# Kernel tuning notes

Measured on AMD Instinct MI355X. Metric: run time of the kernel, lower is better.

Reference implementation:

```python
import jax, jax.numpy as jnp
import numpy as np

DIM = 1024
E = 8
TOP_K = 2
HID = int(DIM * 2.68)  # 2744


def setup_inputs() -> dict:
    key = jax.random.key(0)
    ks = jax.random.split(key, 8)
    s = 0.02
    return {
        "x": jax.random.normal(ks[0], (4, 1024, DIM), dtype=jnp.float32),
        "gate_w": jax.random.normal(ks[1], (E, DIM), dtype=jnp.float32) * s,
        "w1": jax.random.normal(ks[2], (E, HID, DIM), dtype=jnp.float32) * s,
        "w2": jax.random.normal(ks[3], (E, HID, DIM), dtype=jnp.float32) * s,
        "w3": jax.random.normal(ks[4], (E, DIM, HID), dtype=jnp.float32) * s,
        "sw1": jax.random.normal(ks[5], (HID, DIM), dtype=jnp.float32) * s,
        "sw2": jax.random.normal(ks[6], (HID, DIM), dtype=jnp.float32) * s,
        "sw3": jax.random.normal(ks[7], (DIM, HID), dtype=jnp.float32) * s,
    }


def reference(x, gate_w, w1, w2, w3, sw1, sw2, sw3):
    B, T, C = x.shape
    xf = x.reshape(-1, C)  # [S, C]
    logits = xf @ gate_w.T  # [S, E]
    rw = jax.nn.softmax(logits.astype(jnp.float32), axis=-1)
    tkw, tki = jax.lax.top_k(rw, TOP_K)  # [S, K]
    nE = rw.shape[-1]
    importance = rw.mean(0)  # [E]
    load = jax.nn.one_hot(tki[:, 0], nE, dtype=jnp.float32).mean(0)  # [E]
    aux_loss = nE * (importance * load).sum()
    tkw = tkw / tkw.sum(-1, keepdims=True)
    tkw = tkw.astype(x.dtype)
    # dense all-expert SwiGLU (faithful to original: every expert on every token)
    h = jax.nn.silu(jnp.einsum('sc,ehc->seh', xf, w1)) * jnp.einsum('sc,ehc->seh', xf, w2)  # [S,E,H]
    eo = jnp.einsum('seh,ech->sec', h, w3)  # [S, E, C]
    sel = jnp.take_along_axis(eo, tki[:, :, None], axis=1)  # [S, K, C]
    weighted = (sel * tkw[:, :, None]).sum(1)  # [S, C]
    shared = (jax.nn.silu(xf @ sw1.T) * (xf @ sw2.T)) @ sw3.T  # [S, C]
    y = (weighted + shared).reshape(B, T, C)
    return y, aux_loss
```

## Files before the change

kernel.cpp:

```cpp
#include <hip/hip_runtime.h>
#include <cstdio>
#include <cstdint>

#define S_TOK 4096
#define CDIM  1024
#define EXP   8
#define HRAW  2744
#define HPAD  2816
#define MAXROWS  13312
#define MAXTILES 104
#define NSLICE1  (HPAD / 128)
#define NSLICE2  (CDIM / 256)
#define G1_BLKS  (MAXTILES * NSLICE1)

typedef __attribute__((ext_vector_type(8))) short bf16x8;
typedef __attribute__((ext_vector_type(4))) float f32x4;
typedef __attribute__((ext_vector_type(4))) unsigned short us4;
typedef __attribute__((ext_vector_type(8))) unsigned short us8;
typedef unsigned short us;

__device__ __forceinline__ us f2bf(float f) {
  unsigned u = __float_as_uint(f);
  u += 0x7fffu + ((u >> 16) & 1u);
  return (us)(u >> 16);
}
__device__ __forceinline__ float bf2f(us v) {
  return __uint_as_float((unsigned)v << 16);
}

__device__ __forceinline__ void gl16(const us* g, us* l) {
  __builtin_amdgcn_global_load_lds((__attribute__((address_space(1))) void*)g,
                                   (__attribute__((address_space(3))) void*)l,
                                   16, 0, 0);
}

__device__ __forceinline__ int xcd_swz(int orig, int nwg) {
  int q = nwg >> 3, r = nwg & 7;
  int x = orig & 7, idx = orig >> 3;
  return (x < r ? x * (q + 1) : r * (q + 1) + (x - r) * q) + idx;
}

#define CH8_RP1  (HPAD * CDIM / 8)
#define CH8_CPR  (HPAD / 8)

__device__ __forceinline__ void cvt8_rowpad(const float* __restrict__ src,
                                            us* __restrict__ dst, int idx) {
  int m = idx / CH8_RP1, rem = idx - m * CH8_RP1;
  int r = rem >> 7, c8 = rem & 127;
  us8 o;
  if (r < HRAW) {
    const float4* p = (const float4*)(src + ((size_t)(m * HRAW + r) * CDIM + c8 * 8));
    float4 v0 = p[0], v1 = p[1];
    o[0] = f2bf(v0.x); o[1] = f2bf(v0.y); o[2] = f2bf(v0.z); o[3] = f2bf(v0.w);
    o[4] = f2bf(v1.x); o[5] = f2bf(v1.y); o[6] = f2bf(v1.z); o[7] = f2bf(v1.w);
  } else {
    o[0] = 0; o[1] = 0; o[2] = 0; o[3] = 0; o[4] = 0; o[5] = 0; o[6] = 0; o[7] = 0;
  }
  *(us8*)(dst + ((size_t)(m * HPAD + r) * CDIM + c8 * 8)) = o;
}

__device__ __forceinline__ void cvt8_colpad(const float* __restrict__ src,
                                            us* __restrict__ dst, int idx) {
  int r = idx / CH8_CPR, c8 = idx - r * CH8_CPR;
  int c = c8 * 8;
  us8 o;
  if (c < HRAW) {
    const float4* p = (const float4*)(src + (size_t)r * HRAW + c);
    float4 v0 = p[0], v1 = p[1];
    o[0] = f2bf(v0.x); o[1] = f2bf(v0.y); o[2] = f2bf(v0.z); o[3] = f2bf(v0.w);
    o[4] = f2bf(v1.x); o[5] = f2bf(v1.y); o[6] = f2bf(v1.z); o[7] = f2bf(v1.w);
  } else {
    o[0] = 0; o[1] = 0; o[2] = 0; o[3] = 0; o[4] = 0; o[5] = 0; o[6] = 0; o[7] = 0;
  }
  *(us8*)(dst + (size_t)r * HPAD + c) = o;
}

#define GATE_BLKS 1024
#define CVT_BLKS  2048
#define AB8_W1   (8 * CH8_RP1)
#define AB8_W2   (AB8_W1 + 8 * CH8_RP1)
#define AB8_SW1  (AB8_W2 + CH8_RP1)
#define AB8_SW2  (AB8_SW1 + CH8_RP1)

__global__ void __launch_bounds__(256) cvtgate_kernel(
    const float* __restrict__ x, const float* __restrict__ gw,
    const float* __restrict__ w1, const float* __restrict__ w2,
    const float* __restrict__ sw1, const float* __restrict__ sw2,
    us* __restrict__ xb, us* __restrict__ w1b, us* __restrict__ w2b,
    us* __restrict__ sw1b, us* __restrict__ sw2b,
    int* __restrict__ tki, float* __restrict__ tkw, float* __restrict__ probs) {
  if (blockIdx.x < GATE_BLKS) {
    const int wv = threadIdx.x >> 6, lane = threadIdx.x & 63;
    const int s = blockIdx.x * 4 + wv;
    const float4* xs4 = (const float4*)(x + (size_t)s * CDIM);
    float acc[8] = {0, 0, 0, 0, 0, 0, 0, 0};
#pragma unroll
    for (int j = 0; j < 4; j++) {
      float4 v = xs4[lane * 4 + j];
      int c = lane * 16 + j * 4;
      us4 ov;
      ov.x = f2bf(v.x); ov.y = f2bf(v.y); ov.z = f2bf(v.z); ov.w = f2bf(v.w);
      *(us4*)(xb + (size_t)s * CDIM + c) = ov;
#pragma unroll
      for (int ee = 0; ee < 8; ee++) {
        const float* g = gw + ee * CDIM + c;
        acc[ee] += v.x * g[0] + v.y * g[1] + v.z * g[2] + v.w * g[3];
      }
    }
#pragma unroll
    for (int ee = 0; ee < 8; ee++) {
#pragma unroll
      for (int off = 32; off > 0; off >>= 1) acc[ee] += __shfl_xor(acc[ee], off, 64);
    }
    if (lane == 0) {
      float mx = acc[0];
      for (int ee = 1; ee < 8; ee++) mx = fmaxf(mx, acc[ee]);
      float p[8], sm = 0.f;
      for (int ee = 0; ee < 8; ee++) { p[ee] = expf(acc[ee] - mx); sm += p[ee]; }
      float inv = 1.f / sm;
      for (int ee = 0; ee < 8; ee++) probs[s * 8 + ee] = p[ee] * inv;
      int i0 = 0; float b0 = p[0];
      for (int ee = 1; ee < 8; ee++) if (p[ee] > b0) { b0 = p[ee]; i0 = ee; }
      int i1 = -1; float b1 = -1.f;
      for (int ee = 0; ee < 8; ee++) if (ee != i0 && p[ee] > b1) { b1 = p[ee]; i1 = ee; }
      float rw0 = b0 * inv, rw1 = b1 * inv;
      float den = 1.f / (rw0 + rw1);
      tki[2 * s] = i0; tki[2 * s + 1] = i1;
      tkw[2 * s] = rw0 * den; tkw[2 * s + 1] = rw1 * den;
    }
    return;
  }
  for (int i = (blockIdx.x - GATE_BLKS) * 256 + threadIdx.x; i < AB8_SW2;
       i += CVT_BLKS * 256) {
    if (i < AB8_W1)       cvt8_rowpad(w1,  w1b,  i);
    else if (i < AB8_W2)  cvt8_rowpad(w2,  w2b,  i - AB8_W1);
    else if (i < AB8_SW1) cvt8_rowpad(sw1, sw1b, i - AB8_W2);
    else                  cvt8_rowpad(sw2, sw2b, i - AB8_SW1);
  }
}

__global__ void __launch_bounds__(512) build_kernel(const int* __restrict__ tki,
                                                    const float* __restrict__ tkw,
                                                    const float* __restrict__ probs,
                                                    int* __restrict__ meta,
                                                    int* __restrict__ pairtok,
                                                    float* __restrict__ pairw,
                                                    int* __restrict__ invmap,
                                                    int* __restrict__ tile_expert,
                                                    float* __restrict__ aux_out) {
  const int tid = threadIdx.x, lane = tid & 63, wv = tid >> 6;
  __shared__ int s_cnt[EXP];
  __shared__ int s_amc[EXP];
  __shared__ float s_imp[EXP];
  {
    const int e = wv;
    int c_cnt = 0, c_amc = 0;
    float imp = 0.f;
    for (int s0 = 0; s0 < S_TOK; s0 += 64) {
      int s = s0 + lane;
      int i0 = tki[2 * s], i1 = tki[2 * s + 1];
      c_cnt += (i0 == e) || (i1 == e);
      c_amc += (i0 == e);
      imp += probs[s * 8 + e];
    }
#pragma unroll
    for (int off = 32; off > 0; off >>= 1) {
      c_cnt += __shfl_xor(c_cnt, off, 64);
      c_amc += __shfl_xor(c_amc, off, 64);
      imp   += __shfl_xor(imp, off, 64);
    }
    if (lane == 0) { s_cnt[e] = c_cnt; s_amc[e] = c_amc; s_imp[e] = imp; }
  }
  __syncthreads();
  int pad[EXP], start[EXP];
  int o = S_TOK;
#pragma unroll
  for (int j = 0; j < EXP; j++) {
    pad[j] = ((s_cnt[j] + 127) >> 7) << 7;
    start[j] = o;
    o += pad[j];
  }
  const int total = o;
  for (int r = tid; r < S_TOK; r += 512) { pairtok[r] = r; pairw[r] = 1.f; }
  {
    const int e = wv;
    int base = start[e];
    for (int s0 = 0; s0 < S_TOK; s0 += 64) {
      int s = s0 + lane;
      int i0 = tki[2 * s], i1 = tki[2 * s + 1];
      bool m0 = (i0 == e), m1 = (i1 == e);
      bool mm = m0 || m1;
      unsigned long long mk = __ballot(mm);
      if (mm) {
        int pos = base + __popcll(mk & ((1ull << lane) - 1ull));
        pairtok[pos] = s;
        pairw[pos] = m0 ? tkw[2 * s] : tkw[2 * s + 1];
        invmap[2 * s + (m0 ? 0 : 1)] = pos;
      }
      base += __popcll(mk);
    }
    for (int r = base + lane; r < start[e] + pad[e]; r += 64) {
      pairtok[r] = -1; pairw[r] = 0.f;
    }
  }
  if (tid < 128) {
    int ex = 8;
    if (tid >= 32) {
      int rr = tid * 128;
#pragma unroll
      for (int j = 0; j < EXP; j++)
        if (rr >= start[j] && rr < start[j] + pad[j]) ex = j;
    }
    tile_expert[tid] = ex;
  }
  if (tid == 0) {
    meta[0] = total >> 7;
    float a = 0.f;
    for (int j = 0; j < EXP; j++)
      a += (s_imp[j] * (1.f / 4096.f)) * ((float)s_amc[j] * (1.f / 4096.f));
    aux_out[0] = 8.f * a;
  }
}

#define W3CVT_BLKS 1024
#define W38_CHUNKS (8 * CDIM * CH8_CPR)
#define W38_TOT    (W38_CHUNKS + CDIM * CH8_CPR)

__global__ void __launch_bounds__(256, 2) gemm1_kernel(
    const us* __restrict__ xb, const us* __restrict__ w1b, const us* __restrict__ w2b,
    const us* __restrict__ sw1b, const us* __restrict__ sw2b,
    const int* __restrict__ pairtok, const int* __restrict__ tile_expert,
    const int* __restrict__ meta, us* __restrict__ h,
    const float* __restrict__ w3, const float* __restrict__ sw3,
    us* __restrict__ w3b, us* __restrict__ sw3b) {
  if (blockIdx.x >= G1_BLKS) {
    for (int i = (blockIdx.x - G1_BLKS) * 256 + threadIdx.x; i < W38_TOT;
         i += W3CVT_BLKS * 256) {
      if (i < W38_CHUNKS) cvt8_colpad(w3,  w3b,  i);
      else                cvt8_colpad(sw3, sw3b, i - W38_CHUNKS);
    }
    return;
  }
  const int wgid = xcd_swz(blockIdx.x, G1_BLKS);
  const int mt = wgid % MAXTILES;
  if (mt >= meta[0]) return;
  const int n0 = (wgid / MAXTILES) * 128;
  const int e = tile_expert[mt];
  const us* B1 = (e == 8) ? sw1b : (w1b + (size_t)e * HPAD * CDIM);
  const us* B2 = (e == 8) ? sw2b : (w2b + (size_t)e * HPAD * CDIM);
  const int row0 = mt * 128;
  __shared__ __align__(16) us sA[128 * 64];
  __shared__ __align__(16) us sB1[128 * 64];
  __shared__ __align__(16) us sB2[128 * 64];
  const int tid = threadIdx.x, lane = tid & 63;
  const int wm = tid >> 7, wn = (tid >> 6) & 1;
  const int srow = tid >> 3;
  const int soct = (tid & 7) ^ (srow & 7);
  const us* gA[4];
  const us* gB1a[4];
  const us* gB2a[4];
#pragma unroll
  for (int j = 0; j < 4; j++) {
    int t = pairtok[row0 + j * 32 + srow]; if (t < 0) t = 0;
    gA[j]   = xb + (size_t)t * CDIM + soct * 8;
    gB1a[j] = B1 + (size_t)(n0 + j * 32 + srow) * CDIM + soct * 8;
    gB2a[j] = B2 + (size_t)(n0 + j * 32 + srow) * CDIM + soct * 8;
  }
  f32x4 au[4][4], av[4][4];
#pragma unroll
  for (int m = 0; m < 4; m++)
#pragma unroll
    for (int n = 0; n < 4; n++)
#pragma unroll
      for (int r = 0; r < 4; r++) { au[m][n][r] = 0.f; av[m][n][r] = 0.f; }

  const int rl = lane & 15, fo = lane >> 4;
  const int x0 = ((0 + fo) ^ (rl & 7)) << 3;
  const int x1 = ((4 + fo) ^ (rl & 7)) << 3;
  for (int k0 = 0; k0 < CDIM; k0 += 64) {
#pragma unroll
    for (int j = 0; j < 4; j++) {
      gl16(gA[j] + k0,   &sA[(j * 256 + tid) * 8]);
      gl16(gB1a[j] + k0, &sB1[(j * 256 + tid) * 8]);
      gl16(gB2a[j] + k0, &sB2[(j * 256 + tid) * 8]);
    }
    __syncthreads();
#pragma unroll
    for (int ks = 0; ks < 2; ks++) {
      const int kx = ks ? x1 : x0;
      bf16x8 a[4], b1[4], b2[4];
#pragma unroll
      for (int m = 0; m < 4; m++)
        a[m] = *(const bf16x8*)&sA[(wm * 64 + m * 16 + rl) * 64 + kx];
#pragma unroll
      for (int n = 0; n < 4; n++) {
        b1[n] = *(const bf16x8*)&sB1[(wn * 64 + n * 16 + rl) * 64 + kx];
        b2[n] = *(const bf16x8*)&sB2[(wn * 64 + n * 16 + rl) * 64 + kx];
      }
#pragma unroll
      for (int m = 0; m < 4; m++)
#pragma unroll
        for (int n = 0; n < 4; n++) {
          au[m][n] = __builtin_amdgcn_mfma_f32_16x16x32_bf16(a[m], b1[n], au[m][n], 0, 0, 0);
          av[m][n] = __builtin_amdgcn_mfma_f32_16x16x32_bf16(a[m], b2[n], av[m][n], 0, 0, 0);
        }
    }
    __syncthreads();
  }
  const int rb = (lane >> 4) * 4, cb = lane & 15;
#pragma unroll
  for (int m = 0; m < 4; m++)
#pragma unroll
    for (int n = 0; n < 4; n++)
#pragma unroll
      for (int r = 0; r < 4; r++) {
        int row = row0 + wm * 64 + m * 16 + rb + r;
        int col = n0 + wn * 64 + n * 16 + cb;
        float u = au[m][n][r], v = av[m][n][r];
        float sg = 1.f / (1.f + __expf(-u));
        h[(size_t)row * HPAD + col] = f2bf(u * sg * v);
      }
}

__global__ void __launch_bounds__(256, 2) gemm2_kernel(
    const us* __restrict__ h, const us* __restrict__ w3b, const us* __restrict__ sw3b,
    const int* __restrict__ tile_expert, const int* __restrict__ meta,
    us* __restrict__ eo) {
  const int wgid = xcd_swz(blockIdx.x, MAXTILES * NSLICE2);
  const int mt = wgid % MAXTILES;
  if (mt >= meta[0]) return;
  const int n0 = (wgid / MAXTILES) * 256;
  const int e = tile_expert[mt];
  const us* B = (e == 8) ? sw3b : (w3b + (size_t)e * CDIM * HPAD);
  const int row0 = mt * 128;
  __shared__ __align__(16) us sA[128 * 64];
  __shared__ __align__(16) us sB[256 * 64];
  const int tid = threadIdx.x, lane = tid & 63;
  const int wm = tid >> 7, wn = (tid >> 6) & 1;
  const int srow = tid >> 3;
  const int soct = (tid & 7) ^ (srow & 7);
  const us* gA[4];
  const us* gB[8];
#pragma unroll
  for (int j = 0; j < 4; j++)
    gA[j] = h + (size_t)(row0 + j * 32 + srow) * HPAD + soct * 8;
#pragma unroll
  for (int j = 0; j < 8; j++)
    gB[j] = B + (size_t)(n0 + j * 32 + srow) * HPAD + soct * 8;
  f32x4 ac[4][8];
#pragma unroll
  for (int m = 0; m < 4; m++)
#pragma unroll
    for (int n = 0; n < 8; n++)
#pragma unroll
      for (int r = 0; r < 4; r++) ac[m][n][r] = 0.f;

  const int rl = lane & 15, fo = lane >> 4;
  const int x0 = ((0 + fo) ^ (rl & 7)) << 3;
  const int x1 = ((4 + fo) ^ (rl & 7)) << 3;
  for (int k0 = 0; k0 < HPAD; k0 += 64) {
#pragma unroll
    for (int j = 0; j < 4; j++)
      gl16(gA[j] + k0, &sA[(j * 256 + tid) * 8]);
#pragma unroll
    for (int j = 0; j < 8; j++)
      gl16(gB[j] + k0, &sB[(j * 256 + tid) * 8]);
    __syncthreads();
#pragma unroll
    for (int ks = 0; ks < 2; ks++) {
      const int kx = ks ? x1 : x0;
      bf16x8 a[4], b[8];
#pragma unroll
      for (int m = 0; m < 4; m++)
        a[m] = *(const bf16x8*)&sA[(wm * 64 + m * 16 + rl) * 64 + kx];
#pragma unroll
      for (int n = 0; n < 8; n++)
        b[n] = *(const bf16x8*)&sB[(wn * 128 + n * 16 + rl) * 64 + kx];
#pragma unroll
      for (int m = 0; m < 4; m++)
#pragma unroll
        for (int n = 0; n < 8; n++)
          ac[m][n] = __builtin_amdgcn_mfma_f32_16x16x32_bf16(a[m], b[n], ac[m][n], 0, 0, 0);
    }
    __syncthreads();
  }
  const int rb = (lane >> 4) * 4, cb = lane & 15;
#pragma unroll
  for (int m = 0; m < 4; m++)
#pragma unroll
    for (int n = 0; n < 8; n++)
#pragma unroll
      for (int r = 0; r < 4; r++) {
        int row = row0 + wm * 64 + m * 16 + rb + r;
        int col = n0 + wn * 128 + n * 16 + cb;
        eo[(size_t)row * CDIM + col] = f2bf(ac[m][n][r]);
      }
}

__global__ void __launch_bounds__(256) combine_kernel(const us* __restrict__ eo,
                                                      const int* __restrict__ invmap,
                                                      const float* __restrict__ pairw,
                                                      float* __restrict__ out) {
  const int s = blockIdx.x;
  const int c = threadIdx.x * 4;
  const int j0 = invmap[2 * s], j1 = invmap[2 * s + 1];
  const float w0 = pairw[j0], w1 = pairw[j1];
  us4 a = *(const us4*)(eo + (size_t)s * CDIM + c);
  us4 b = *(const us4*)(eo + (size_t)j0 * CDIM + c);
  us4 d = *(const us4*)(eo + (size_t)j1 * CDIM + c);
  float4 o;
  o.x = bf2f(a.x) + w0 * bf2f(b.x) + w1 * bf2f(d.x);
  o.y = bf2f(a.y) + w0 * bf2f(b.y) + w1 * bf2f(d.y);
  o.z = bf2f(a.z) + w0 * bf2f(b.z) + w1 * bf2f(d.z);
  o.w = bf2f(a.w) + w0 * bf2f(b.w) + w1 * bf2f(d.w);
  *(float4*)(out + (size_t)s * CDIM + c) = o;
}

extern "C" void kernel_launch(void* const* d_in, const int* in_sizes, int n_in,
                              void* d_out, int out_size, void* d_ws, size_t ws_size,
                              hipStream_t stream) {
  const float* x   = (const float*)d_in[0];
  const float* gw  = (const float*)d_in[1];
  const float* w1  = (const float*)d_in[2];
  const float* w2  = (const float*)d_in[3];
  const float* w3  = (const float*)d_in[4];
  const float* sw1 = (const float*)d_in[5];
  const float* sw2 = (const float*)d_in[6];
  const float* sw3 = (const float*)d_in[7];
  float* out = (float*)d_out;
  char* ws = (char*)d_ws;
  size_t off = 0;
  auto take = [&](size_t bytes) -> char* {
    char* p = ws + off;
    off = (off + bytes + 255) & ~(size_t)255;
    return p;
  };
  us* xb    = (us*)take((size_t)S_TOK * CDIM * 2);
  us* w1b   = (us*)take((size_t)EXP * HPAD * CDIM * 2);
  us* w2b   = (us*)take((size_t)EXP * HPAD * CDIM * 2);
  us* w3b   = (us*)take((size_t)EXP * CDIM * HPAD * 2);
  us* sw1b  = (us*)take((size_t)HPAD * CDIM * 2);
  us* sw2b  = (us*)take((size_t)HPAD * CDIM * 2);
  us* sw3b  = (us*)take((size_t)CDIM * HPAD * 2);
  us* hbuf  = (us*)take((size_t)MAXROWS * HPAD * 2);
  us* eo    = (us*)take((size_t)MAXROWS * CDIM * 2);
  int* pairtok = (int*)take(MAXROWS * 4);
  float* pairw = (float*)take(MAXROWS * 4);
  int* invmap  = (int*)take(S_TOK * 2 * 4);
  int* tile_expert = (int*)take(128 * 4);
  int* tki = (int*)take(S_TOK * 2 * 4);
  float* tkw = (float*)take(S_TOK * 2 * 4);
  float* probs = (float*)take(S_TOK * EXP * 4);
  int* meta = (int*)take(256);
  if (off > ws_size) {
    fprintf(stderr, "MoE kernel: ws too small, need %zu got %zu\n", off, ws_size);
    return;
  }
  cvtgate_kernel<<<GATE_BLKS + CVT_BLKS, 256, 0, stream>>>(
      x, gw, w1, w2, sw1, sw2, xb, w1b, w2b, sw1b, sw2b, tki, tkw, probs);
  build_kernel<<<1, 512, 0, stream>>>(tki, tkw, probs, meta, pairtok, pairw, invmap,
                                      tile_expert, out + (size_t)S_TOK * CDIM);
  gemm1_kernel<<<G1_BLKS + W3CVT_BLKS, 256, 0, stream>>>(
      xb, w1b, w2b, sw1b, sw2b, pairtok, tile_expert, meta, hbuf,
      w3, sw3, w3b, sw3b);
  gemm2_kernel<<<MAXTILES * NSLICE2, 256, 0, stream>>>(
      hbuf, w3b, sw3b, tile_expert, meta, eo);
  combine_kernel<<<S_TOK, 256, 0, stream>>>(eo, invmap, pairw, out);
}
```

Baseline: 409.4 us.

## Double-buffer gemm2 with 256x256 tiles and overlap routing build with weight conversion

Splits gating into its own kernel and folds the single-block routing build into the weight-conversion kernel, so the build runs alongside conversion instead of as a serial launch. Expert segments are now padded to 256 rows, so gemm2 can use 512-thread blocks with 256x256 tiles and double-buffered LDS that prefetches the next K slice while MFMAs run, with priority hints. Both GEMMs now skip tiles whose first row is padding. Larger padding adds wasted rows and more workspace, and the bigger gemm2 tile yields fewer blocks, which may lower occupancy.

```diff
diff --git a/kernel.cpp b/kernel.cpp
--- a/kernel.cpp
+++ b/kernel.cpp
@@ -7,11 +7,13 @@
 #define EXP   8
 #define HRAW  2744
 #define HPAD  2816
-#define MAXROWS  13312
-#define MAXTILES 104
+#define MAXROWS  14336
+#define MAXTILES 112
+#define MAXT2    56
 #define NSLICE1  (HPAD / 128)
-#define NSLICE2  (CDIM / 256)
 #define G1_BLKS  (MAXTILES * NSLICE1)
+#define G2_BLKS  (MAXT2 * 4)
+#define NT2K     (HPAD / 64)
 
 typedef __attribute__((ext_vector_type(8))) short bf16x8;
 typedef __attribute__((ext_vector_type(4))) float f32x4;
@@ -75,150 +77,149 @@
   *(us8*)(dst + (size_t)r * HPAD + c) = o;
 }
 
-#define GATE_BLKS 1024
-#define CVT_BLKS  2048
+__global__ void __launch_bounds__(256) gate_kernel(const float* __restrict__ x,
+                                                   const float* __restrict__ gw,
+                                                   us* __restrict__ xb,
+                                                   int* __restrict__ tki,
+                                                   float* __restrict__ tkw,
+                                                   float* __restrict__ probs) {
+  const int wv = threadIdx.x >> 6, lane = threadIdx.x & 63;
+  const int s = blockIdx.x * 4 + wv;
+  const float4* xs4 = (const float4*)(x + (size_t)s * CDIM);
+  float acc[8] = {0, 0, 0, 0, 0, 0, 0, 0};
+#pragma unroll
+  for (int j = 0; j < 4; j++) {
+    float4 v = xs4[lane * 4 + j];
+    int c = lane * 16 + j * 4;
+    us4 ov;
+    ov.x = f2bf(v.x); ov.y = f2bf(v.y); ov.z = f2bf(v.z); ov.w = f2bf(v.w);
+    *(us4*)(xb + (size_t)s * CDIM + c) = ov;
+#pragma unroll
+    for (int ee = 0; ee < 8; ee++) {
+      const float* g = gw + ee * CDIM + c;
+      acc[ee] += v.x * g[0] + v.y * g[1] + v.z * g[2] + v.w * g[3];
+    }
+  }
+#pragma unroll
+  for (int ee = 0; ee < 8; ee++) {
+#pragma unroll
+    for (int off = 32; off > 0; off >>= 1) acc[ee] += __shfl_xor(acc[ee], off, 64);
+  }
+  if (lane == 0) {
+    float mx = acc[0];
+    for (int ee = 1; ee < 8; ee++) mx = fmaxf(mx, acc[ee]);
+    float p[8], sm = 0.f;
+    for (int ee = 0; ee < 8; ee++) { p[ee] = expf(acc[ee] - mx); sm += p[ee]; }
+    float inv = 1.f / sm;
+    for (int ee = 0; ee < 8; ee++) probs[s * 8 + ee] = p[ee] * inv;
+    int i0 = 0; float b0 = p[0];
+    for (int ee = 1; ee < 8; ee++) if (p[ee] > b0) { b0 = p[ee]; i0 = ee; }
+    int i1 = -1; float b1 = -1.f;
+    for (int ee = 0; ee < 8; ee++) if (ee != i0 && p[ee] > b1) { b1 = p[ee]; i1 = ee; }
+    float rw0 = b0 * inv, rw1 = b1 * inv;
+    float den = 1.f / (rw0 + rw1);
+    tki[2 * s] = i0; tki[2 * s + 1] = i1;
+    tkw[2 * s] = rw0 * den; tkw[2 * s + 1] = rw1 * den;
+  }
+}
+
+#define CVTAB_BLKS 2048
 #define AB8_W1   (8 * CH8_RP1)
 #define AB8_W2   (AB8_W1 + 8 * CH8_RP1)
 #define AB8_SW1  (AB8_W2 + CH8_RP1)
 #define AB8_SW2  (AB8_SW1 + CH8_RP1)
 
-__global__ void __launch_bounds__(256) cvtgate_kernel(
-    const float* __restrict__ x, const float* __restrict__ gw,
+__global__ void __launch_bounds__(512) cvtab_build_kernel(
     const float* __restrict__ w1, const float* __restrict__ w2,
     const float* __restrict__ sw1, const float* __restrict__ sw2,
-    us* __restrict__ xb, us* __restrict__ w1b, us* __restrict__ w2b,
+    us* __restrict__ w1b, us* __restrict__ w2b,
     us* __restrict__ sw1b, us* __restrict__ sw2b,
-    int* __restrict__ tki, float* __restrict__ tkw, float* __restrict__ probs) {
-  if (blockIdx.x < GATE_BLKS) {
-    const int wv = threadIdx.x >> 6, lane = threadIdx.x & 63;
-    const int s = blockIdx.x * 4 + wv;
-    const float4* xs4 = (const float4*)(x + (size_t)s * CDIM);
-    float acc[8] = {0, 0, 0, 0, 0, 0, 0, 0};
-#pragma unroll
-    for (int j = 0; j < 4; j++) {
-      float4 v = xs4[lane * 4 + j];
-      int c = lane * 16 + j * 4;
-      us4 ov;
-      ov.x = f2bf(v.x); ov.y = f2bf(v.y); ov.z = f2bf(v.z); ov.w = f2bf(v.w);
-      *(us4*)(xb + (size_t)s * CDIM + c) = ov;
-#pragma unroll
-      for (int ee = 0; ee < 8; ee++) {
-        const float* g = gw + ee * CDIM + c;
-        acc[ee] += v.x * g[0] + v.y * g[1] + v.z * g[2] + v.w * g[3];
-      }
-    }
-#pragma unroll
-    for (int ee = 0; ee < 8; ee++) {
-#pragma unroll
-      for (int off = 32; off > 0; off >>= 1) acc[ee] += __shfl_xor(acc[ee], off, 64);
-    }
-    if (lane == 0) {
-      float mx = acc[0];
-      for (int ee = 1; ee < 8; ee++) mx = fmaxf(mx, acc[ee]);
-      float p[8], sm = 0.f;
-      for (int ee = 0; ee < 8; ee++) { p[ee] = expf(acc[ee] - mx); sm += p[ee]; }
-      float inv = 1.f / sm;
-      for (int ee = 0; ee < 8; ee++) probs[s * 8 + ee] = p[ee] * inv;
-      int i0 = 0; float b0 = p[0];
-      for (int ee = 1; ee < 8; ee++) if (p[ee] > b0) { b0 = p[ee]; i0 = ee; }
-      int i1 = -1; float b1 = -1.f;
-      for (int ee = 0; ee < 8; ee++) if (ee != i0 && p[ee] > b1) { b1 = p[ee]; i1 = ee; }
-      float rw0 = b0 * inv, rw1 = b1 * inv;
-      float den = 1.f / (rw0 + rw1);
-      tki[2 * s] = i0; tki[2 * s + 1] = i1;
-      tkw[2 * s] = rw0 * den; tkw[2 * s + 1] = rw1 * den;
+    const int* __restrict__ tki, const float* __restrict__ tkw,
+    const float* __restrict__ probs, int* __restrict__ meta,
+    int* __restrict__ pairtok, float* __restrict__ pairw,
+    int* __restrict__ invmap, int* __restrict__ tile_expert,
+    float* __restrict__ aux_out) {
+  if (blockIdx.x == 0) {
+    const int tid = threadIdx.x, lane = tid & 63, wv = tid >> 6;
+    __shared__ int s_cnt[EXP];
+    __shared__ int s_amc[EXP];
+    __shared__ float s_imp[EXP];
+    {
+      const int e = wv;
+      int c_cnt = 0, c_amc = 0;
+      float imp = 0.f;
+      for (int s0 = 0; s0 < S_TOK; s0 += 64) {
+        int s = s0 + lane;
+        int i0 = tki[2 * s], i1 = tki[2 * s + 1];
+        c_cnt += (i0 == e) || (i1 == e);
+        c_amc += (i0 == e);
+        imp += probs[s * 8 + e];
+      }
+#pragma unroll
+      for (int off = 32; off > 0; off >>= 1) {
+        c_cnt += __shfl_xor(c_cnt, off, 64);
+        c_amc += __shfl_xor(c_amc, off, 64);
+        imp   += __shfl_xor(imp, off, 64);
+      }
+      if (lane == 0) { s_cnt[e] = c_cnt; s_amc[e] = c_amc; s_imp[e] = imp; }
+    }
+    __syncthreads();
+    int pad[EXP], start[EXP];
+    int o = S_TOK;
+#pragma unroll
+    for (int j = 0; j < EXP; j++) {
+      pad[j] = ((s_cnt[j] + 255) >> 8) << 8;
+      start[j] = o;
+      o += pad[j];
+    }
+    const int total = o;
+    for (int r = tid; r < S_TOK; r += 512) { pairtok[r] = r; pairw[r] = 1.f; }
+    {
+      const int e = wv;
+      int base = start[e];
+      for (int s0 = 0; s0 < S_TOK; s0 += 64) {
+        int s = s0 + lane;
+        int i0 = tki[2 * s], i1 = tki[2 * s + 1];
+        bool m0 = (i0 == e), m1 = (i1 == e);
+        bool mm = m0 || m1;
+        unsigned long long mk = __ballot(mm);
+        if (mm) {
+          int pos = base + __popcll(mk & ((1ull << lane) - 1ull));
+          pairtok[pos] = s;
+          pairw[pos] = m0 ? tkw[2 * s] : tkw[2 * s + 1];
+          invmap[2 * s + (m0 ? 0 : 1)] = pos;
+        }
+        base += __popcll(mk);
+      }
+      for (int r = base + lane; r < start[e] + pad[e]; r += 64) {
+        pairtok[r] = -1; pairw[r] = 0.f;
+      }
+    }
+    if (tid < 128) {
+      int ex = 8;
+      if (tid >= 32) {
+        int rr = tid * 128;
+#pragma unroll
+        for (int j = 0; j < EXP; j++)
+          if (rr >= start[j] && rr < start[j] + pad[j]) ex = j;
+      }
+      tile_expert[tid] = ex;
+    }
+    if (tid == 0) {
+      meta[0] = total >> 7;
+      float a = 0.f;
+      for (int j = 0; j < EXP; j++)
+        a += (s_imp[j] * (1.f / 4096.f)) * ((float)s_amc[j] * (1.f / 4096.f));
+      aux_out[0] = 8.f * a;
     }
     return;
   }
-  for (int i = (blockIdx.x - GATE_BLKS) * 256 + threadIdx.x; i < AB8_SW2;
-       i += CVT_BLKS * 256) {
+  for (int i = (blockIdx.x - 1) * 512 + threadIdx.x; i < AB8_SW2;
+       i += (CVTAB_BLKS - 1) * 512) {
     if (i < AB8_W1)       cvt8_rowpad(w1,  w1b,  i);
     else if (i < AB8_W2)  cvt8_rowpad(w2,  w2b,  i - AB8_W1);
     else if (i < AB8_SW1) cvt8_rowpad(sw1, sw1b, i - AB8_W2);
     else                  cvt8_rowpad(sw2, sw2b, i - AB8_SW1);
-  }
-}
-
-__global__ void __launch_bounds__(512) build_kernel(const int* __restrict__ tki,
-                                                    const float* __restrict__ tkw,
-                                                    const float* __restrict__ probs,
-                                                    int* __restrict__ meta,
-                                                    int* __restrict__ pairtok,
-                                                    float* __restrict__ pairw,
-                                                    int* __restrict__ invmap,
-                                                    int* __restrict__ tile_expert,
-                                                    float* __restrict__ aux_out) {
-  const int tid = threadIdx.x, lane = tid & 63, wv = tid >> 6;
-  __shared__ int s_cnt[EXP];
-  __shared__ int s_amc[EXP];
-  __shared__ float s_imp[EXP];
-  {
-    const int e = wv;
-    int c_cnt = 0, c_amc = 0;
-    float imp = 0.f;
-    for (int s0 = 0; s0 < S_TOK; s0 += 64) {
-      int s = s0 + lane;
-      int i0 = tki[2 * s], i1 = tki[2 * s + 1];
-      c_cnt += (i0 == e) || (i1 == e);
-      c_amc += (i0 == e);
-      imp += probs[s * 8 + e];
-    }
-#pragma unroll
-    for (int off = 32; off > 0; off >>= 1) {
-      c_cnt += __shfl_xor(c_cnt, off, 64);
-      c_amc += __shfl_xor(c_amc, off, 64);
-      imp   += __shfl_xor(imp, off, 64);
-    }
-    if (lane == 0) { s_cnt[e] = c_cnt; s_amc[e] = c_amc; s_imp[e] = imp; }
-  }
-  __syncthreads();
-  int pad[EXP], start[EXP];
-  int o = S_TOK;
-#pragma unroll
-  for (int j = 0; j < EXP; j++) {
-    pad[j] = ((s_cnt[j] + 127) >> 7) << 7;
-    start[j] = o;
-    o += pad[j];
-  }
-  const int total = o;
-  for (int r = tid; r < S_TOK; r += 512) { pairtok[r] = r; pairw[r] = 1.f; }
-  {
-    const int e = wv;
-    int base = start[e];
-    for (int s0 = 0; s0 < S_TOK; s0 += 64) {
-      int s = s0 + lane;
-      int i0 = tki[2 * s], i1 = tki[2 * s + 1];
-      bool m0 = (i0 == e), m1 = (i1 == e);
-      bool mm = m0 || m1;
-      unsigned long long mk = __ballot(mm);
-      if (mm) {
-        int pos = base + __popcll(mk & ((1ull << lane) - 1ull));
-        pairtok[pos] = s;
-        pairw[pos] = m0 ? tkw[2 * s] : tkw[2 * s + 1];
-        invmap[2 * s + (m0 ? 0 : 1)] = pos;
-      }
-      base += __popcll(mk);
-    }
-    for (int r = base + lane; r < start[e] + pad[e]; r += 64) {
-      pairtok[r] = -1; pairw[r] = 0.f;
-    }
-  }
-  if (tid < 128) {
-    int ex = 8;
-    if (tid >= 32) {
-      int rr = tid * 128;
-#pragma unroll
-      for (int j = 0; j < EXP; j++)
-        if (rr >= start[j] && rr < start[j] + pad[j]) ex = j;
-    }
-    tile_expert[tid] = ex;
-  }
-  if (tid == 0) {
-    meta[0] = total >> 7;
-    float a = 0.f;
-    for (int j = 0; j < EXP; j++)
-      a += (s_imp[j] * (1.f / 4096.f)) * ((float)s_amc[j] * (1.f / 4096.f));
-    aux_out[0] = 8.f * a;
   }
 }
 
@@ -244,11 +245,12 @@
   const int wgid = xcd_swz(blockIdx.x, G1_BLKS);
   const int mt = wgid % MAXTILES;
   if (mt >= meta[0]) return;
+  const int row0 = mt * 128;
+  if (pairtok[row0] < 0) return;
   const int n0 = (wgid / MAXTILES) * 128;
   const int e = tile_expert[mt];
   const us* B1 = (e == 8) ? sw1b : (w1b + (size_t)e * HPAD * CDIM);
   const us* B2 = (e == 8) ? sw2b : (w2b + (size_t)e * HPAD * CDIM);
-  const int row0 = mt * 128;
   __shared__ __align__(16) us sA[128 * 64];
   __shared__ __align__(16) us sB1[128 * 64];
   __shared__ __align__(16) us sB2[128 * 64];
@@ -322,77 +324,92 @@
       }
 }
 
-__global__ void __launch_bounds__(256, 2) gemm2_kernel(
+__global__ void __launch_bounds__(512, 2) gemm2_kernel(
     const us* __restrict__ h, const us* __restrict__ w3b, const us* __restrict__ sw3b,
-    const int* __restrict__ tile_expert, const int* __restrict__ meta,
-    us* __restrict__ eo) {
-  const int wgid = xcd_swz(blockIdx.x, MAXTILES * NSLICE2);
-  const int mt = wgid % MAXTILES;
-  if (mt >= meta[0]) return;
-  const int n0 = (wgid / MAXTILES) * 256;
-  const int e = tile_expert[mt];
+    const int* __restrict__ pairtok, const int* __restrict__ tile_expert,
+    const int* __restrict__ meta, us* __restrict__ eo) {
+  const int wgid = xcd_swz(blockIdx.x, G2_BLKS);
+  const int mt2 = wgid % MAXT2;
+  if (2 * mt2 >= meta[0]) return;
+  const int row0 = mt2 * 256;
+  if (pairtok[row0] < 0) return;
+  const int n0 = (wgid / MAXT2) * 256;
+  const int e = tile_expert[2 * mt2];
   const us* B = (e == 8) ? sw3b : (w3b + (size_t)e * CDIM * HPAD);
-  const int row0 = mt * 128;
-  __shared__ __align__(16) us sA[128 * 64];
-  __shared__ __align__(16) us sB[256 * 64];
+  __shared__ __align__(16) us sA[2][256 * 64];
+  __shared__ __align__(16) us sB[2][256 * 64];
   const int tid = threadIdx.x, lane = tid & 63;
-  const int wm = tid >> 7, wn = (tid >> 6) & 1;
+  const int wid = tid >> 6, wm = wid >> 2, wn = wid & 3;
   const int srow = tid >> 3;
   const int soct = (tid & 7) ^ (srow & 7);
   const us* gA[4];
-  const us* gB[8];
-#pragma unroll
-  for (int j = 0; j < 4; j++)
-    gA[j] = h + (size_t)(row0 + j * 32 + srow) * HPAD + soct * 8;
-#pragma unroll
-  for (int j = 0; j < 8; j++)
-    gB[j] = B + (size_t)(n0 + j * 32 + srow) * HPAD + soct * 8;
-  f32x4 ac[4][8];
-#pragma unroll
-  for (int m = 0; m < 4; m++)
-#pragma unroll
-    for (int n = 0; n < 8; n++)
+  const us* gB[4];
+#pragma unroll
+  for (int j = 0; j < 4; j++) {
+    gA[j] = h + (size_t)(row0 + j * 64 + srow) * HPAD + soct * 8;
+    gB[j] = B + (size_t)(n0 + j * 64 + srow) * HPAD + soct * 8;
+  }
+  f32x4 ac[8][4];
+#pragma unroll
+  for (int m = 0; m < 8; m++)
+#pragma unroll
+    for (int n = 0; n < 4; n++)
 #pragma unroll
       for (int r = 0; r < 4; r++) ac[m][n][r] = 0.f;
 
   const int rl = lane & 15, fo = lane >> 4;
-  const int x0 = ((0 + fo) ^ (rl & 7)) << 3;
-  const int x1 = ((4 + fo) ^ (rl & 7)) << 3;
-  for (int k0 = 0; k0 < HPAD; k0 += 64) {
-#pragma unroll
-    for (int j = 0; j < 4; j++)
-      gl16(gA[j] + k0, &sA[(j * 256 + tid) * 8]);
-#pragma unroll
-    for (int j = 0; j < 8; j++)
-      gl16(gB[j] + k0, &sB[(j * 256 + tid) * 8]);
-    __syncthreads();
-#pragma unroll
-    for (int ks = 0; ks < 2; ks++) {
-      const int kx = ks ? x1 : x0;
-      bf16x8 a[4], b[8];
+#pragma unroll
+  for (int j = 0; j < 4; j++) {
+    gl16(gA[j], &sA[0][j * 4096 + tid * 8]);
+    gl16(gB[j], &sB[0][j * 4096 + tid * 8]);
+  }
+  asm volatile("s_waitcnt vmcnt(0)" ::: "memory");
+  __builtin_amdgcn_s_barrier();
+#pragma unroll 1
+  for (int t = 0; t < NT2K; t++) {
+    const int slot = t & 1;
+    const int k1 = (t + 1) * 64;
+    const us* pa = sA[slot];
+    const us* pb = sB[slot];
+#pragma unroll
+    for (int p = 0; p < 4; p++) {
+      const int ks = p >> 1, mh = p & 1;
+      const int kx = (((ks << 2) + fo) ^ (rl & 7)) << 3;
+      bf16x8 a[4], b[4];
 #pragma unroll
       for (int m = 0; m < 4; m++)
-        a[m] = *(const bf16x8*)&sA[(wm * 64 + m * 16 + rl) * 64 + kx];
-#pragma unroll
-      for (int n = 0; n < 8; n++)
-        b[n] = *(const bf16x8*)&sB[(wn * 128 + n * 16 + rl) * 64 + kx];
+        a[m] = *(const bf16x8*)&pa[(wm * 128 + mh * 64 + m * 16 + rl) * 64 + kx];
+#pragma unroll
+      for (int n = 0; n < 4; n++)
+        b[n] = *(const bf16x8*)&pb[(wn * 64 + n * 16 + rl) * 64 + kx];
+      if (t + 1 < NT2K) {
+        gl16(gA[p] + k1, &sA[slot ^ 1][p * 4096 + tid * 8]);
+        gl16(gB[p] + k1, &sB[slot ^ 1][p * 4096 + tid * 8]);
+      }
+      asm volatile("s_waitcnt lgkmcnt(0)" ::: "memory");
+      __builtin_amdgcn_sched_barrier(0);
+      __builtin_amdgcn_s_setprio(1);
 #pragma unroll
       for (int m = 0; m < 4; m++)
 #pragma unroll
-        for (int n = 0; n < 8; n++)
-          ac[m][n] = __builtin_amdgcn_mfma_f32_16x16x32_bf16(a[m], b[n], ac[m][n], 0, 0, 0);
-    }
-    __syncthreads();
+        for (int n = 0; n < 4; n++)
+          ac[mh * 4 + m][n] =
+              __builtin_amdgcn_mfma_f32_16x16x32_bf16(a[m], b[n], ac[mh * 4 + m][n], 0, 0, 0);
+      __builtin_amdgcn_s_setprio(0);
+      __builtin_amdgcn_s_barrier();
+    }
+    asm volatile("s_waitcnt vmcnt(0)" ::: "memory");
+    __builtin_amdgcn_s_barrier();
   }
   const int rb = (lane >> 4) * 4, cb = lane & 15;
 #pragma unroll
-  for (int m = 0; m < 4; m++)
-#pragma unroll
-    for (int n = 0; n < 8; n++)
+  for (int m = 0; m < 8; m++)
+#pragma unroll
+    for (int n = 0; n < 4; n++)
 #pragma unroll
       for (int r = 0; r < 4; r++) {
-        int row = row0 + wm * 64 + m * 16 + rb + r;
-        int col = n0 + wn * 128 + n * 16 + cb;
+        int row = row0 + wm * 128 + m * 16 + rb + r;
+        int col = n0 + wn * 64 + n * 16 + cb;
         eo[(size_t)row * CDIM + col] = f2bf(ac[m][n][r]);
       }
 }
@@ -456,14 +473,15 @@
     fprintf(stderr, "MoE kernel: ws too small, need %zu got %zu\n", off, ws_size);
     return;
   }
-  cvtgate_kernel<<<GATE_BLKS + CVT_BLKS, 256, 0, stream>>>(
-      x, gw, w1, w2, sw1, sw2, xb, w1b, w2b, sw1b, sw2b, tki, tkw, probs);
-  build_kernel<<<1, 512, 0, stream>>>(tki, tkw, probs, meta, pairtok, pairw, invmap,
-                                      tile_expert, out + (size_t)S_TOK * CDIM);
+  gate_kernel<<<S_TOK / 4, 256, 0, stream>>>(x, gw, xb, tki, tkw, probs);
+  cvtab_build_kernel<<<CVTAB_BLKS, 512, 0, stream>>>(
+      w1, w2, sw1, sw2, w1b, w2b, sw1b, sw2b,
+      tki, tkw, probs, meta, pairtok, pairw, invmap, tile_expert,
+      out + (size_t)S_TOK * CDIM);
   gemm1_kernel<<<G1_BLKS + W3CVT_BLKS, 256, 0, stream>>>(
       xb, w1b, w2b, sw1b, sw2b, pairtok, tile_expert, meta, hbuf,
       w3, sw3, w3b, sw3b);
-  gemm2_kernel<<<MAXTILES * NSLICE2, 256, 0, stream>>>(
-      hbuf, w3b, sw3b, tile_expert, meta, eo);
+  gemm2_kernel<<<G2_BLKS, 512, 0, stream>>>(
+      hbuf, w3b, sw3b, pairtok, tile_expert, meta, eo);
   combine_kernel<<<S_TOK, 256, 0, stream>>>(eo, invmap, pairw, out);
 }
```

Result: no change. 414.0 us (+1.1%).
